# Kernel tuning notes

Hardware: AMD Instinct MI355X
Metric: run time of the kernel (lower is better)

The kernel has to match this reference:

```python
import jax, jax.numpy as jnp
import numpy as np

B, S, H = 2, 2048, 1024
I = 1024          # moe_intermediate_size
E = 8             # n_routed_experts
K = 2             # num_experts_per_tok
SCALE = 1.0       # routed_scaling_factor


def setup_inputs() -> dict:
    key = jax.random.key(0)
    ks = jax.random.split(key, 8)
    sd = 1.0 / np.sqrt(H)
    si = 1.0 / np.sqrt(I)
    return {
        "hidden_states": jax.random.normal(ks[0], (B, S, H), jnp.float32),
        "router_w": jax.random.uniform(ks[1], (E, H), jnp.float32, -sd, sd),
        # shared expert (n_shared_experts = 1); weights stored [in, out]
        "shared_gate": jax.random.uniform(ks[2], (H, I), jnp.float32, -sd, sd),
        "shared_up": jax.random.uniform(ks[3], (H, I), jnp.float32, -sd, sd),
        "shared_down": jax.random.uniform(ks[4], (I, H), jnp.float32, -si, si),
        # routed experts, stacked [E, in, out]
        "experts_gate": jax.random.uniform(ks[5], (E, H, I), jnp.float32, -sd, sd),
        "experts_up": jax.random.uniform(ks[6], (E, H, I), jnp.float32, -sd, sd),
        "experts_down": jax.random.uniform(ks[7], (E, I, H), jnp.float32, -si, si),
    }


def reference(hidden_states, router_w, shared_gate, shared_up, shared_down,
              experts_gate, experts_up, experts_down):
    residual = hidden_states
    x = hidden_states.reshape(-1, H)                      # [T, H], T = B*S

    # shared expert (SwiGLU-ish: sigmoid(gate) * up)
    sg = x @ shared_gate
    su = x @ shared_up
    shared_out = (jax.nn.sigmoid(sg) * su) @ shared_down  # [T, H]

    # router: softmax over experts, greedy top-k
    logits = x @ router_w.T                               # [T, E]
    scores = jax.nn.softmax(logits.astype(jnp.float32), axis=-1)
    topk_w, topk_idx = jax.lax.top_k(scores, K)           # [T, K]
    topk_w = topk_w * SCALE

    # dense compute of ALL experts on all tokens (faithful to reference)
    g = jnp.einsum('th,ehi->tei', x, experts_gate)        # [T, E, I]
    u = jnp.einsum('th,ehi->tei', x, experts_up)
    hid = jax.nn.sigmoid(g) * u
    expert_outputs = jnp.einsum('tei,eih->teh', hid, experts_down)  # [T, E, H]

    # gather top-k expert outputs and combine
    selected = jnp.take_along_axis(expert_outputs, topk_idx[:, :, None], axis=1)  # [T, K, H]
    routed_out = (selected * topk_w[:, :, None]).sum(axis=1)                      # [T, H]

    out = residual + (shared_out + routed_out).reshape(B, S, H)
    return out
```

## Files before the change

kernel.cpp:

```cpp
#include <hip/hip_runtime.h>
#include <hip/hip_bf16.h>

#define T_TOK 4096
#define HDIM 1024
#define IDIM 1024
#define EDIM 8

typedef __attribute__((ext_vector_type(8))) short bf16x8;
typedef __attribute__((ext_vector_type(4))) float f32x4;

static __device__ __forceinline__ unsigned short f2bf(float f) {
  union { float f; unsigned int u; } v; v.f = f;
  unsigned int u = v.u;
  unsigned int r = u + 0x7FFFu + ((u >> 16) & 1u);
  return (unsigned short)(r >> 16);
}

#define GLD16(g, l) __builtin_amdgcn_global_load_lds( \
    (const __attribute__((address_space(1))) void*)(g), \
    (__attribute__((address_space(3))) void*)(l), 16, 0, 0)

__global__ __launch_bounds__(256) void convert_x(const float4* __restrict__ x4,
                                                 ushort4* __restrict__ xb4) {
  int i = blockIdx.x * 256 + threadIdx.x;
  float4 v = x4[i];
  ushort4 o;
  o.x = f2bf(v.x); o.y = f2bf(v.y); o.z = f2bf(v.z); o.w = f2bf(v.w);
  xb4[i] = o;
}

__global__ void zero_cnt(int* __restrict__ cnt) {
  if (threadIdx.x < 16) cnt[threadIdx.x] = 0;
}

struct SrcPtrs { const float* p[6]; };

__global__ __launch_bounds__(256) void transpose_all(SrcPtrs S,
                                                     unsigned short* __restrict__ dstBase) {
  __shared__ unsigned short t[32][36];
  const int z = blockIdx.z;
  const float* src;
  if (z == 0)       src = S.p[0];
  else if (z == 1)  src = S.p[1];
  else if (z == 2)  src = S.p[2];
  else if (z < 11)  src = S.p[3] + (size_t)(z - 3)  * 1048576;
  else if (z < 19)  src = S.p[4] + (size_t)(z - 11) * 1048576;
  else              src = S.p[5] + (size_t)(z - 19) * 1048576;
  unsigned short* dst = dstBase + (size_t)z * 1048576;

  const int r0 = blockIdx.y * 32;
  const int c0 = blockIdx.x * 32;
  const int tid = threadIdx.x;
  const int rr = tid >> 3;
  const int cc = (tid & 7) * 4;
  const float4 v = *(const float4*)&src[(size_t)(r0 + rr) * 1024 + c0 + cc];
  t[rr][cc + 0] = f2bf(v.x); t[rr][cc + 1] = f2bf(v.y);
  t[rr][cc + 2] = f2bf(v.z); t[rr][cc + 3] = f2bf(v.w);
  __syncthreads();
  const int n = rr;
  const int k4 = cc;
  ushort4 o;
  o.x = t[k4 + 0][n]; o.y = t[k4 + 1][n]; o.z = t[k4 + 2][n]; o.w = t[k4 + 3][n];
  *(ushort4*)&dst[(size_t)(c0 + n) * 1024 + r0 + k4] = o;
}

__global__ __launch_bounds__(256) void router2(
    const float* __restrict__ x, const float* __restrict__ rw,
    int* __restrict__ cnt, int* __restrict__ list, float* __restrict__ wgt) {
  __shared__ float rwT[1024 * 8];
  const int tid = threadIdx.x;
#pragma unroll
  for (int c = 0; c < 4; c++) {
    const int h = c * 256 + tid;
    float v[8];
#pragma unroll
    for (int e = 0; e < EDIM; e++) v[e] = rw[e * 1024 + h];
    *(float4*)&rwT[h * 8]     = make_float4(v[0], v[1], v[2], v[3]);
    *(float4*)&rwT[h * 8 + 4] = make_float4(v[4], v[5], v[6], v[7]);
  }
  __syncthreads();

  const int tt = tid >> 4;
  const int pp = tid & 15;
  const int t = blockIdx.x * 16 + tt;
  const float* xr = x + (size_t)t * HDIM;

  float a[EDIM];
#pragma unroll
  for (int e = 0; e < EDIM; e++) a[e] = 0.f;

#pragma unroll 8
  for (int i = 0; i < 64; i++) {
    const int h = pp + 16 * i;
    const float xs = xr[h];
    const float4 r0 = *(const float4*)&rwT[h * 8];
    const float4 r1 = *(const float4*)&rwT[h * 8 + 4];
    a[0] += xs * r0.x; a[1] += xs * r0.y; a[2] += xs * r0.z; a[3] += xs * r0.w;
    a[4] += xs * r1.x; a[5] += xs * r1.y; a[6] += xs * r1.z; a[7] += xs * r1.w;
  }
#pragma unroll
  for (int s = 1; s < 16; s <<= 1) {
#pragma unroll
    for (int e = 0; e < EDIM; e++) a[e] += __shfl_xor(a[e], s, 16);
  }
  if (pp == 0) {
    float m = a[0];
#pragma unroll
    for (int e = 1; e < EDIM; e++) m = fmaxf(m, a[e]);
    float p[EDIM]; float s = 0.f;
#pragma unroll
    for (int e = 0; e < EDIM; e++) { p[e] = expf(a[e] - m); s += p[e]; }
    float inv = 1.f / s;
    int e1 = 0; float b1 = p[0];
#pragma unroll
    for (int e = 1; e < EDIM; e++) if (p[e] > b1) { b1 = p[e]; e1 = e; }
    int e2 = -1; float b2 = -1.f;
#pragma unroll
    for (int e = 0; e < EDIM; e++) if (e != e1 && p[e] > b2) { b2 = p[e]; e2 = e; }
    int pos1 = atomicAdd(&cnt[e1], 1);
    list[e1 * T_TOK + pos1] = t; wgt[e1 * T_TOK + pos1] = b1 * inv;
    int pos2 = atomicAdd(&cnt[e2], 1);
    list[e2 * T_TOK + pos2] = t; wgt[e2 * T_TOK + pos2] = b2 * inv;
  }
}

template <bool GATHER>
__global__ __launch_bounds__(256) void gateup_gemm(
    const unsigned short* __restrict__ xb,
    const unsigned short* __restrict__ WgT_, const unsigned short* __restrict__ WuT_,
    unsigned short* __restrict__ hid,
    const int* __restrict__ cnt, const int* __restrict__ list) {
  __shared__ unsigned short Al[128 * 64];
  __shared__ unsigned short Bg[64 * 64];
  __shared__ unsigned short Bu[64 * 64];

  const int tid = threadIdx.x;
  const int lane = tid & 63;
  const int w = tid >> 6;
  const int wm = w >> 1, wn = w & 1;

  int count, hidbase, e = 0;
  const unsigned short *wg, *wu;
  if constexpr (GATHER) {
    e = blockIdx.z;
    count = cnt[e];
    if ((int)blockIdx.y * 128 >= count) return;
    int off = 0;
#pragma unroll
    for (int i = 0; i < EDIM; i++) off += (i < e) ? cnt[i] : 0;
    hidbase = off;
    wg = WgT_ + (size_t)e * HDIM * IDIM;
    wu = WuT_ + (size_t)e * HDIM * IDIM;
  } else {
    count = T_TOK; hidbase = 0; wg = WgT_; wu = WuT_;
  }
  const int m0 = blockIdx.y * 128;
  const int n0 = blockIdx.x * 64;

  const unsigned short* gA[4];
  unsigned short* lA[4];
#pragma unroll
  for (int j = 0; j < 4; j++) {
    const int s = w * 256 + j * 64 + lane;
    const int row = s >> 3;
    const int cg = (s & 7) ^ (row & 7);
    int tok;
    if constexpr (GATHER) {
      int p = m0 + row; if (p >= count) p = count - 1;
      tok = list[e * T_TOK + p];
    } else {
      tok = m0 + row;
    }
    gA[j] = xb + (size_t)tok * HDIM + cg * 8;
    lA[j] = &Al[(w * 256 + j * 64) * 8];
  }
  const unsigned short *gG[2], *gU[2];
  unsigned short *lG[2], *lU[2];
#pragma unroll
  for (int j = 0; j < 2; j++) {
    const int s = w * 128 + j * 64 + lane;
    const int row = s >> 3;
    const int cg = (s & 7) ^ (row & 7);
    gG[j] = wg + (size_t)(n0 + row) * HDIM + cg * 8;
    gU[j] = wu + (size_t)(n0 + row) * HDIM + cg * 8;
    lG[j] = &Bg[(w * 128 + j * 64) * 8];
    lU[j] = &Bu[(w * 128 + j * 64) * 8];
  }

  f32x4 accg[4][2], accu[4][2];
  const f32x4 z4 = {0.f, 0.f, 0.f, 0.f};
#pragma unroll
  for (int i = 0; i < 4; i++)
#pragma unroll
    for (int j = 0; j < 2; j++) { accg[i][j] = z4; accu[i][j] = z4; }

  const int q = lane >> 4;
  const int r16 = lane & 15;
  const int rx = r16 & 7;

  for (int k0 = 0; k0 < HDIM; k0 += 64) {
    __syncthreads();
#pragma unroll
    for (int j = 0; j < 4; j++) GLD16(gA[j] + k0, lA[j]);
#pragma unroll
    for (int j = 0; j < 2; j++) { GLD16(gG[j] + k0, lG[j]); GLD16(gU[j] + k0, lU[j]); }
    __syncthreads();

    bf16x8 af[4][2], bg2[2][2], bu2[2][2];
#pragma unroll
    for (int h = 0; h < 2; h++) {
      const int ch = ((h * 4 + q) ^ rx) * 8;
#pragma unroll
      for (int i = 0; i < 4; i++)
        af[i][h] = *(const bf16x8*)&Al[(wm * 64 + i * 16 + r16) * 64 + ch];
#pragma unroll
      for (int j = 0; j < 2; j++) {
        bg2[j][h] = *(const bf16x8*)&Bg[(wn * 32 + j * 16 + r16) * 64 + ch];
        bu2[j][h] = *(const bf16x8*)&Bu[(wn * 32 + j * 16 + r16) * 64 + ch];
      }
    }
#pragma unroll
    for (int h = 0; h < 2; h++)
#pragma unroll
      for (int i = 0; i < 4; i++)
#pragma unroll
        for (int j = 0; j < 2; j++) {
          accg[i][j] = __builtin_amdgcn_mfma_f32_16x16x32_bf16(af[i][h], bg2[j][h], accg[i][j], 0, 0, 0);
          accu[i][j] = __builtin_amdgcn_mfma_f32_16x16x32_bf16(af[i][h], bu2[j][h], accu[i][j], 0, 0, 0);
        }
  }

#pragma unroll
  for (int i = 0; i < 4; i++) {
#pragma unroll
    for (int j = 0; j < 2; j++) {
      const int col = n0 + wn * 32 + j * 16 + r16;
#pragma unroll
      for (int r = 0; r < 4; r++) {
        int pos = m0 + wm * 64 + i * 16 + q * 4 + r;
        bool ok = GATHER ? (pos < count) : true;
        if (ok) {
          float g = accg[i][j][r], u = accu[i][j][r];
          float h = u / (1.f + __expf(-g));
          hid[(size_t)(hidbase + pos) * IDIM + col] = f2bf(h);
        }
      }
    }
  }
}

template <bool ROUTED>
__global__ __launch_bounds__(256) void down_gemm(
    const unsigned short* __restrict__ hidin,
    const unsigned short* __restrict__ WdT_,
    float* __restrict__ out, const float* __restrict__ resid,
    const int* __restrict__ cnt, const int* __restrict__ list,
    const float* __restrict__ wgt) {
  __shared__ unsigned short Al[128 * 64];
  __shared__ unsigned short Bl[128 * 64];

  const int tid = threadIdx.x;
  const int lane = tid & 63;
  const int w = tid >> 6;
  const int wm = w >> 1, wn = w & 1;

  int count, abase, e = 0;
  const unsigned short* wd;
  if constexpr (ROUTED) {
    e = blockIdx.z;
    count = cnt[e];
    if ((int)blockIdx.y * 128 >= count) return;
    int off = 0;
#pragma unroll
    for (int i = 0; i < EDIM; i++) off += (i < e) ? cnt[i] : 0;
    abase = off;
    wd = WdT_ + (size_t)e * IDIM * HDIM;
  } else {
    count = T_TOK; abase = 0; wd = WdT_;
  }
  const int m0 = blockIdx.y * 128;
  const int n0 = blockIdx.x * 128;

  const unsigned short *gA[4], *gB[4];
  unsigned short *lA[4], *lB[4];
#pragma unroll
  for (int j = 0; j < 4; j++) {
    const int s = w * 256 + j * 64 + lane;
    const int row = s >> 3;
    const int cg = (s & 7) ^ (row & 7);
    gA[j] = hidin + (size_t)(abase + m0 + row) * IDIM + cg * 8;
    gB[j] = wd + (size_t)(n0 + row) * IDIM + cg * 8;
    lA[j] = &Al[(w * 256 + j * 64) * 8];
    lB[j] = &Bl[(w * 256 + j * 64) * 8];
  }

  f32x4 acc[4][4];
  const f32x4 z4 = {0.f, 0.f, 0.f, 0.f};
#pragma unroll
  for (int i = 0; i < 4; i++)
#pragma unroll
    for (int j = 0; j < 4; j++) acc[i][j] = z4;

  const int q = lane >> 4;
  const int r16 = lane & 15;
  const int rx = r16 & 7;

  for (int k0 = 0; k0 < IDIM; k0 += 64) {
    __syncthreads();
#pragma unroll
    for (int j = 0; j < 4; j++) GLD16(gA[j] + k0, lA[j]);
#pragma unroll
    for (int j = 0; j < 4; j++) GLD16(gB[j] + k0, lB[j]);
    __syncthreads();

    bf16x8 af[4][2], bf4[4][2];
#pragma unroll
    for (int h = 0; h < 2; h++) {
      const int ch = ((h * 4 + q) ^ rx) * 8;
#pragma unroll
      for (int i = 0; i < 4; i++)
        af[i][h] = *(const bf16x8*)&Al[(wm * 64 + i * 16 + r16) * 64 + ch];
#pragma unroll
      for (int j = 0; j < 4; j++)
        bf4[j][h] = *(const bf16x8*)&Bl[(wn * 64 + j * 16 + r16) * 64 + ch];
    }
#pragma unroll
    for (int h = 0; h < 2; h++)
#pragma unroll
      for (int i = 0; i < 4; i++)
#pragma unroll
        for (int j = 0; j < 4; j++)
          acc[i][j] = __builtin_amdgcn_mfma_f32_16x16x32_bf16(af[i][h], bf4[j][h], acc[i][j], 0, 0, 0);
  }

#pragma unroll
  for (int i = 0; i < 4; i++) {
    int toks[4]; float ws4[4];
#pragma unroll
    for (int r = 0; r < 4; r++) {
      int pos = m0 + wm * 64 + i * 16 + q * 4 + r;
      if constexpr (ROUTED) {
        bool ok = pos < count;
        toks[r] = ok ? list[e * T_TOK + pos] : -1;
        ws4[r] = ok ? wgt[e * T_TOK + pos] : 0.f;
      } else {
        toks[r] = pos; ws4[r] = 1.f;
      }
    }
#pragma unroll
    for (int j = 0; j < 4; j++) {
      const int col = n0 + wn * 64 + j * 16 + r16;
#pragma unroll
      for (int r = 0; r < 4; r++) {
        if constexpr (ROUTED) {
          if (toks[r] >= 0)
            atomicAdd(&out[(size_t)toks[r] * HDIM + col], ws4[r] * acc[i][j][r]);
        } else {
          size_t idx = (size_t)toks[r] * HDIM + col;
          out[idx] = resid[idx] + acc[i][j][r];
        }
      }
    }
  }
}

extern "C" void kernel_launch(void* const* d_in, const int* in_sizes, int n_in,
                              void* d_out, int out_size, void* d_ws, size_t ws_size,
                              hipStream_t stream) {
  const float* x  = (const float*)d_in[0];
  const float* rw = (const float*)d_in[1];
  const float* sg = (const float*)d_in[2];
  const float* su = (const float*)d_in[3];
  const float* sd = (const float*)d_in[4];
  const float* eg = (const float*)d_in[5];
  const float* eu = (const float*)d_in[6];
  const float* ed = (const float*)d_in[7];
  float* out = (float*)d_out;

  char* ws = (char*)d_ws;
  unsigned short* xb   = (unsigned short*)ws;
  unsigned short* shid = xb + (size_t)T_TOK * HDIM;
  unsigned short* rhid = shid + (size_t)T_TOK * IDIM;
  int*   cnt  = (int*)(rhid + (size_t)(T_TOK * 2 + 128) * IDIM);
  int*   list = cnt + 16;
  float* wgt  = (float*)(list + EDIM * T_TOK);
  unsigned short* wT = (unsigned short*)(wgt + EDIM * T_TOK);
  unsigned short* sgT = wT;
  unsigned short* suT = sgT + (size_t)HDIM * IDIM;
  unsigned short* sdT = suT + (size_t)HDIM * IDIM;
  unsigned short* egT = sdT + (size_t)IDIM * HDIM;
  unsigned short* euT = egT + (size_t)EDIM * HDIM * IDIM;
  unsigned short* edT = euT + (size_t)EDIM * HDIM * IDIM;

  zero_cnt<<<1, 64, 0, stream>>>(cnt);
  convert_x<<<(T_TOK * HDIM) / 1024, 256, 0, stream>>>((const float4*)x, (ushort4*)xb);
  router2<<<T_TOK / 16, 256, 0, stream>>>(x, rw, cnt, list, wgt);

  SrcPtrs S; S.p[0] = sg; S.p[1] = su; S.p[2] = sd; S.p[3] = eg; S.p[4] = eu; S.p[5] = ed;
  transpose_all<<<dim3(32, 32, 27), 256, 0, stream>>>(S, wT);

  gateup_gemm<false><<<dim3(IDIM / 64, T_TOK / 128, 1), 256, 0, stream>>>(
      xb, sgT, suT, shid, nullptr, nullptr);
  gateup_gemm<true><<<dim3(IDIM / 64, T_TOK / 128, EDIM), 256, 0, stream>>>(
      xb, egT, euT, rhid, cnt, list);

  down_gemm<false><<<dim3(HDIM / 128, T_TOK / 128, 1), 256, 0, stream>>>(
      shid, sdT, out, x, nullptr, nullptr, nullptr);
  down_gemm<true><<<dim3(HDIM / 128, T_TOK / 128, EDIM), 256, 0, stream>>>(
      rhid, edT, out, nullptr, cnt, list, wgt);
}
```

Baseline: 391.1 us.

## Merge shared and routed expert GEMMs into single launches with double-buffered K=32 stages

Treats the shared expert as a ninth expert so gate/up and down each run as one grid launch instead of two, and reorders the transposed weight layout to match. The GEMM main loops now use a 2-stage LDS double buffer with 32-wide K slices, so the next tile's global-to-LDS loads overlap the current tile's MFMAs. The residual is copied into the output during x conversion, and the shared down GEMM now accumulates with atomics instead of plain stores. This removes launch gaps and exposed load latency, at the cost of more atomic traffic and smaller per-stage K tiles.

```diff
diff --git a/kernel.cpp b/kernel.cpp
--- a/kernel.cpp
+++ b/kernel.cpp
@@ -5,6 +5,7 @@
 #define HDIM 1024
 #define IDIM 1024
 #define EDIM 8
+#define HID_SHARED_BASE 8320
 
 typedef __attribute__((ext_vector_type(8))) short bf16x8;
 typedef __attribute__((ext_vector_type(4))) float f32x4;
@@ -21,9 +22,11 @@
     (__attribute__((address_space(3))) void*)(l), 16, 0, 0)
 
 __global__ __launch_bounds__(256) void convert_x(const float4* __restrict__ x4,
-                                                 ushort4* __restrict__ xb4) {
+                                                 ushort4* __restrict__ xb4,
+                                                 float4* __restrict__ out4) {
   int i = blockIdx.x * 256 + threadIdx.x;
   float4 v = x4[i];
+  out4[i] = v;
   ushort4 o;
   o.x = f2bf(v.x); o.y = f2bf(v.y); o.z = f2bf(v.z); o.w = f2bf(v.w);
   xb4[i] = o;
@@ -39,14 +42,14 @@
                                                      unsigned short* __restrict__ dstBase) {
   __shared__ unsigned short t[32][36];
   const int z = blockIdx.z;
-  const float* src;
-  if (z == 0)       src = S.p[0];
-  else if (z == 1)  src = S.p[1];
-  else if (z == 2)  src = S.p[2];
-  else if (z < 11)  src = S.p[3] + (size_t)(z - 3)  * 1048576;
-  else if (z < 19)  src = S.p[4] + (size_t)(z - 11) * 1048576;
-  else              src = S.p[5] + (size_t)(z - 19) * 1048576;
-  unsigned short* dst = dstBase + (size_t)z * 1048576;
+  const float* src; int dz;
+  if (z == 0)      { src = S.p[0];                              dz = 8;  }
+  else if (z == 1) { src = S.p[1];                              dz = 17; }
+  else if (z == 2) { src = S.p[2];                              dz = 26; }
+  else if (z < 11) { src = S.p[3] + (size_t)(z - 3)  * 1048576; dz = z - 3; }
+  else if (z < 19) { src = S.p[4] + (size_t)(z - 11) * 1048576; dz = 9 + (z - 11); }
+  else             { src = S.p[5] + (size_t)(z - 19) * 1048576; dz = 18 + (z - 19); }
+  unsigned short* dst = dstBase + (size_t)dz * 1048576;
 
   const int r0 = blockIdx.y * 32;
   const int c0 = blockIdx.x * 32;
@@ -57,11 +60,9 @@
   t[rr][cc + 0] = f2bf(v.x); t[rr][cc + 1] = f2bf(v.y);
   t[rr][cc + 2] = f2bf(v.z); t[rr][cc + 3] = f2bf(v.w);
   __syncthreads();
-  const int n = rr;
-  const int k4 = cc;
   ushort4 o;
-  o.x = t[k4 + 0][n]; o.y = t[k4 + 1][n]; o.z = t[k4 + 2][n]; o.w = t[k4 + 3][n];
-  *(ushort4*)&dst[(size_t)(c0 + n) * 1024 + r0 + k4] = o;
+  o.x = t[cc + 0][rr]; o.y = t[cc + 1][rr]; o.z = t[cc + 2][rr]; o.w = t[cc + 3][rr];
+  *(ushort4*)&dst[(size_t)(c0 + rr) * 1024 + r0 + cc] = o;
 }
 
 __global__ __launch_bounds__(256) void router2(
@@ -124,68 +125,57 @@
   }
 }
 
-template <bool GATHER>
-__global__ __launch_bounds__(256) void gateup_gemm(
+__global__ __launch_bounds__(256) void gateup_f(
     const unsigned short* __restrict__ xb,
-    const unsigned short* __restrict__ WgT_, const unsigned short* __restrict__ WuT_,
+    const unsigned short* __restrict__ gateT,
+    const unsigned short* __restrict__ upT,
     unsigned short* __restrict__ hid,
     const int* __restrict__ cnt, const int* __restrict__ list) {
-  __shared__ unsigned short Al[128 * 64];
-  __shared__ unsigned short Bg[64 * 64];
-  __shared__ unsigned short Bu[64 * 64];
+  __shared__ unsigned short Al[2][128 * 32];
+  __shared__ unsigned short Bg[2][64 * 32];
+  __shared__ unsigned short Bu[2][64 * 32];
 
   const int tid = threadIdx.x;
   const int lane = tid & 63;
   const int w = tid >> 6;
   const int wm = w >> 1, wn = w & 1;
-
-  int count, hidbase, e = 0;
-  const unsigned short *wg, *wu;
-  if constexpr (GATHER) {
-    e = blockIdx.z;
-    count = cnt[e];
-    if ((int)blockIdx.y * 128 >= count) return;
-    int off = 0;
-#pragma unroll
-    for (int i = 0; i < EDIM; i++) off += (i < e) ? cnt[i] : 0;
-    hidbase = off;
-    wg = WgT_ + (size_t)e * HDIM * IDIM;
-    wu = WuT_ + (size_t)e * HDIM * IDIM;
-  } else {
-    count = T_TOK; hidbase = 0; wg = WgT_; wu = WuT_;
-  }
+  const int z = blockIdx.z;
   const int m0 = blockIdx.y * 128;
   const int n0 = blockIdx.x * 64;
 
-  const unsigned short* gA[4];
-  unsigned short* lA[4];
-#pragma unroll
-  for (int j = 0; j < 4; j++) {
-    const int s = w * 256 + j * 64 + lane;
-    const int row = s >> 3;
-    const int cg = (s & 7) ^ (row & 7);
-    int tok;
-    if constexpr (GATHER) {
-      int p = m0 + row; if (p >= count) p = count - 1;
-      tok = list[e * T_TOK + p];
-    } else {
-      tok = m0 + row;
-    }
-    gA[j] = xb + (size_t)tok * HDIM + cg * 8;
-    lA[j] = &Al[(w * 256 + j * 64) * 8];
-  }
-  const unsigned short *gG[2], *gU[2];
-  unsigned short *lG[2], *lU[2];
+  int count, hidbase;
+  if (z < EDIM) {
+    count = cnt[z];
+    if (m0 >= count) return;
+    int off = 0;
+#pragma unroll
+    for (int i = 0; i < EDIM; i++) off += (i < z) ? cnt[i] : 0;
+    hidbase = off;
+  } else {
+    count = T_TOK;
+    hidbase = HID_SHARED_BASE;
+  }
+  const unsigned short* wg = gateT + (size_t)z * HDIM * IDIM;
+  const unsigned short* wu = upT   + (size_t)z * HDIM * IDIM;
+
+  const unsigned short* gA[2];
 #pragma unroll
   for (int j = 0; j < 2; j++) {
     const int s = w * 128 + j * 64 + lane;
-    const int row = s >> 3;
-    const int cg = (s & 7) ^ (row & 7);
-    gG[j] = wg + (size_t)(n0 + row) * HDIM + cg * 8;
-    gU[j] = wu + (size_t)(n0 + row) * HDIM + cg * 8;
-    lG[j] = &Bg[(w * 128 + j * 64) * 8];
-    lU[j] = &Bu[(w * 128 + j * 64) * 8];
-  }
+    const int row = s >> 2;
+    const int g = (s & 3) ^ ((row + (row >> 2)) & 3);
+    int tok;
+    if (z < EDIM) {
+      int p = m0 + row; if (p >= count) p = count - 1;
+      tok = list[z * T_TOK + p];
+    } else tok = m0 + row;
+    gA[j] = xb + (size_t)tok * HDIM + g * 8;
+  }
+  const int sB = w * 64 + lane;
+  const int rowB = sB >> 2;
+  const int gB = (sB & 3) ^ ((rowB + (rowB >> 2)) & 3);
+  const unsigned short* gGp = wg + (size_t)(n0 + rowB) * HDIM + gB * 8;
+  const unsigned short* gUp = wu + (size_t)(n0 + rowB) * HDIM + gB * 8;
 
   f32x4 accg[4][2], accu[4][2];
   const f32x4 z4 = {0.f, 0.f, 0.f, 0.f};
@@ -196,38 +186,42 @@
 
   const int q = lane >> 4;
   const int r16 = lane & 15;
-  const int rx = r16 & 7;
-
-  for (int k0 = 0; k0 < HDIM; k0 += 64) {
+  const int ch = (q ^ ((r16 + (r16 >> 2)) & 3)) * 8;
+
+  auto stage = [&](int k0, int b) {
+    GLD16(gA[0] + k0, &Al[b][(w * 128) * 8]);
+    GLD16(gA[1] + k0, &Al[b][(w * 128 + 64) * 8]);
+    GLD16(gGp + k0, &Bg[b][(w * 64) * 8]);
+    GLD16(gUp + k0, &Bu[b][(w * 64) * 8]);
+  };
+  auto compute = [&](int b) {
+    bf16x8 af[4], bg2[2], bu2[2];
+#pragma unroll
+    for (int i = 0; i < 4; i++)
+      af[i] = *(const bf16x8*)&Al[b][(wm * 64 + i * 16 + r16) * 32 + ch];
+#pragma unroll
+    for (int j = 0; j < 2; j++) {
+      bg2[j] = *(const bf16x8*)&Bg[b][(wn * 32 + j * 16 + r16) * 32 + ch];
+      bu2[j] = *(const bf16x8*)&Bu[b][(wn * 32 + j * 16 + r16) * 32 + ch];
+    }
+#pragma unroll
+    for (int i = 0; i < 4; i++)
+#pragma unroll
+      for (int j = 0; j < 2; j++) {
+        accg[i][j] = __builtin_amdgcn_mfma_f32_16x16x32_bf16(af[i], bg2[j], accg[i][j], 0, 0, 0);
+        accu[i][j] = __builtin_amdgcn_mfma_f32_16x16x32_bf16(af[i], bu2[j], accu[i][j], 0, 0, 0);
+      }
+  };
+
+  stage(0, 0);
+#pragma unroll 1
+  for (int p = 0; p < 16; p++) {
     __syncthreads();
-#pragma unroll
-    for (int j = 0; j < 4; j++) GLD16(gA[j] + k0, lA[j]);
-#pragma unroll
-    for (int j = 0; j < 2; j++) { GLD16(gG[j] + k0, lG[j]); GLD16(gU[j] + k0, lU[j]); }
+    stage((2 * p + 1) * 32, 1);
+    compute(0);
     __syncthreads();
-
-    bf16x8 af[4][2], bg2[2][2], bu2[2][2];
-#pragma unroll
-    for (int h = 0; h < 2; h++) {
-      const int ch = ((h * 4 + q) ^ rx) * 8;
-#pragma unroll
-      for (int i = 0; i < 4; i++)
-        af[i][h] = *(const bf16x8*)&Al[(wm * 64 + i * 16 + r16) * 64 + ch];
-#pragma unroll
-      for (int j = 0; j < 2; j++) {
-        bg2[j][h] = *(const bf16x8*)&Bg[(wn * 32 + j * 16 + r16) * 64 + ch];
-        bu2[j][h] = *(const bf16x8*)&Bu[(wn * 32 + j * 16 + r16) * 64 + ch];
-      }
-    }
-#pragma unroll
-    for (int h = 0; h < 2; h++)
-#pragma unroll
-      for (int i = 0; i < 4; i++)
-#pragma unroll
-        for (int j = 0; j < 2; j++) {
-          accg[i][j] = __builtin_amdgcn_mfma_f32_16x16x32_bf16(af[i][h], bg2[j][h], accg[i][j], 0, 0, 0);
-          accu[i][j] = __builtin_amdgcn_mfma_f32_16x16x32_bf16(af[i][h], bu2[j][h], accu[i][j], 0, 0, 0);
-        }
+    if (p < 15) stage((2 * p + 2) * 32, 0);
+    compute(1);
   }
 
 #pragma unroll
@@ -238,8 +232,7 @@
 #pragma unroll
       for (int r = 0; r < 4; r++) {
         int pos = m0 + wm * 64 + i * 16 + q * 4 + r;
-        bool ok = GATHER ? (pos < count) : true;
-        if (ok) {
+        if (pos < count) {
           float g = accg[i][j][r], u = accu[i][j][r];
           float h = u / (1.f + __expf(-g));
           hid[(size_t)(hidbase + pos) * IDIM + col] = f2bf(h);
@@ -249,49 +242,45 @@
   }
 }
 
-template <bool ROUTED>
-__global__ __launch_bounds__(256) void down_gemm(
-    const unsigned short* __restrict__ hidin,
-    const unsigned short* __restrict__ WdT_,
-    float* __restrict__ out, const float* __restrict__ resid,
+__global__ __launch_bounds__(256) void down_f(
+    const unsigned short* __restrict__ hid,
+    const unsigned short* __restrict__ downT,
+    float* __restrict__ out,
     const int* __restrict__ cnt, const int* __restrict__ list,
     const float* __restrict__ wgt) {
-  __shared__ unsigned short Al[128 * 64];
-  __shared__ unsigned short Bl[128 * 64];
+  __shared__ unsigned short Al[2][128 * 32];
+  __shared__ unsigned short Bl[2][128 * 32];
 
   const int tid = threadIdx.x;
   const int lane = tid & 63;
   const int w = tid >> 6;
   const int wm = w >> 1, wn = w & 1;
-
-  int count, abase, e = 0;
-  const unsigned short* wd;
-  if constexpr (ROUTED) {
-    e = blockIdx.z;
-    count = cnt[e];
-    if ((int)blockIdx.y * 128 >= count) return;
-    int off = 0;
-#pragma unroll
-    for (int i = 0; i < EDIM; i++) off += (i < e) ? cnt[i] : 0;
-    abase = off;
-    wd = WdT_ + (size_t)e * IDIM * HDIM;
-  } else {
-    count = T_TOK; abase = 0; wd = WdT_;
-  }
+  const int z = blockIdx.z;
   const int m0 = blockIdx.y * 128;
   const int n0 = blockIdx.x * 128;
 
-  const unsigned short *gA[4], *gB[4];
-  unsigned short *lA[4], *lB[4];
-#pragma unroll
-  for (int j = 0; j < 4; j++) {
-    const int s = w * 256 + j * 64 + lane;
-    const int row = s >> 3;
-    const int cg = (s & 7) ^ (row & 7);
-    gA[j] = hidin + (size_t)(abase + m0 + row) * IDIM + cg * 8;
-    gB[j] = wd + (size_t)(n0 + row) * IDIM + cg * 8;
-    lA[j] = &Al[(w * 256 + j * 64) * 8];
-    lB[j] = &Bl[(w * 256 + j * 64) * 8];
+  int count, abase;
+  if (z < EDIM) {
+    count = cnt[z];
+    if (m0 >= count) return;
+    int off = 0;
+#pragma unroll
+    for (int i = 0; i < EDIM; i++) off += (i < z) ? cnt[i] : 0;
+    abase = off;
+  } else {
+    count = T_TOK;
+    abase = HID_SHARED_BASE;
+  }
+  const unsigned short* wd = downT + (size_t)z * IDIM * HDIM;
+
+  const unsigned short *gA[2], *gBp[2];
+#pragma unroll
+  for (int j = 0; j < 2; j++) {
+    const int s = w * 128 + j * 64 + lane;
+    const int row = s >> 2;
+    const int g = (s & 3) ^ ((row + (row >> 2)) & 3);
+    gA[j]  = hid + (size_t)(abase + m0 + row) * IDIM + g * 8;
+    gBp[j] = wd + (size_t)(n0 + row) * IDIM + g * 8;
   }
 
   f32x4 acc[4][4];
@@ -303,34 +292,38 @@
 
   const int q = lane >> 4;
   const int r16 = lane & 15;
-  const int rx = r16 & 7;
-
-  for (int k0 = 0; k0 < IDIM; k0 += 64) {
+  const int ch = (q ^ ((r16 + (r16 >> 2)) & 3)) * 8;
+
+  auto stage = [&](int k0, int b) {
+    GLD16(gA[0] + k0,  &Al[b][(w * 128) * 8]);
+    GLD16(gA[1] + k0,  &Al[b][(w * 128 + 64) * 8]);
+    GLD16(gBp[0] + k0, &Bl[b][(w * 128) * 8]);
+    GLD16(gBp[1] + k0, &Bl[b][(w * 128 + 64) * 8]);
+  };
+  auto compute = [&](int b) {
+    bf16x8 af[4], bf4[4];
+#pragma unroll
+    for (int i = 0; i < 4; i++)
+      af[i] = *(const bf16x8*)&Al[b][(wm * 64 + i * 16 + r16) * 32 + ch];
+#pragma unroll
+    for (int j = 0; j < 4; j++)
+      bf4[j] = *(const bf16x8*)&Bl[b][(wn * 64 + j * 16 + r16) * 32 + ch];
+#pragma unroll
+    for (int i = 0; i < 4; i++)
+#pragma unroll
+      for (int j = 0; j < 4; j++)
+        acc[i][j] = __builtin_amdgcn_mfma_f32_16x16x32_bf16(af[i], bf4[j], acc[i][j], 0, 0, 0);
+  };
+
+  stage(0, 0);
+#pragma unroll 1
+  for (int p = 0; p < 16; p++) {
     __syncthreads();
-#pragma unroll
-    for (int j = 0; j < 4; j++) GLD16(gA[j] + k0, lA[j]);
-#pragma unroll
-    for (int j = 0; j < 4; j++) GLD16(gB[j] + k0, lB[j]);
+    stage((2 * p + 1) * 32, 1);
+    compute(0);
     __syncthreads();
-
-    bf16x8 af[4][2], bf4[4][2];
-#pragma unroll
-    for (int h = 0; h < 2; h++) {
-      const int ch = ((h * 4 + q) ^ rx) * 8;
-#pragma unroll
-      for (int i = 0; i < 4; i++)
-        af[i][h] = *(const bf16x8*)&Al[(wm * 64 + i * 16 + r16) * 64 + ch];
-#pragma unroll
-      for (int j = 0; j < 4; j++)
-        bf4[j][h] = *(const bf16x8*)&Bl[(wn * 64 + j * 16 + r16) * 64 + ch];
-    }
-#pragma unroll
-    for (int h = 0; h < 2; h++)
-#pragma unroll
-      for (int i = 0; i < 4; i++)
-#pragma unroll
-        for (int j = 0; j < 4; j++)
-          acc[i][j] = __builtin_amdgcn_mfma_f32_16x16x32_bf16(af[i][h], bf4[j][h], acc[i][j], 0, 0, 0);
+    if (p < 15) stage((2 * p + 2) * 32, 0);
+    compute(1);
   }
 
 #pragma unroll
@@ -339,10 +332,10 @@
 #pragma unroll
     for (int r = 0; r < 4; r++) {
       int pos = m0 + wm * 64 + i * 16 + q * 4 + r;
-      if constexpr (ROUTED) {
+      if (z < EDIM) {
         bool ok = pos < count;
-        toks[r] = ok ? list[e * T_TOK + pos] : -1;
-        ws4[r] = ok ? wgt[e * T_TOK + pos] : 0.f;
+        toks[r] = ok ? list[z * T_TOK + pos] : -1;
+        ws4[r] = ok ? wgt[z * T_TOK + pos] : 0.f;
       } else {
         toks[r] = pos; ws4[r] = 1.f;
       }
@@ -352,13 +345,8 @@
       const int col = n0 + wn * 64 + j * 16 + r16;
 #pragma unroll
       for (int r = 0; r < 4; r++) {
-        if constexpr (ROUTED) {
-          if (toks[r] >= 0)
-            atomicAdd(&out[(size_t)toks[r] * HDIM + col], ws4[r] * acc[i][j][r]);
-        } else {
-          size_t idx = (size_t)toks[r] * HDIM + col;
-          out[idx] = resid[idx] + acc[i][j][r];
-        }
+        if (toks[r] >= 0)
+          atomicAdd(&out[(size_t)toks[r] * HDIM + col], ws4[r] * acc[i][j][r]);
       }
     }
   }
@@ -378,34 +366,24 @@
   float* out = (float*)d_out;
 
   char* ws = (char*)d_ws;
-  unsigned short* xb   = (unsigned short*)ws;
-  unsigned short* shid = xb + (size_t)T_TOK * HDIM;
-  unsigned short* rhid = shid + (size_t)T_TOK * IDIM;
-  int*   cnt  = (int*)(rhid + (size_t)(T_TOK * 2 + 128) * IDIM);
+  unsigned short* xb  = (unsigned short*)ws;
+  unsigned short* hid = xb + (size_t)T_TOK * HDIM;
+  int*   cnt  = (int*)(hid + (size_t)(HID_SHARED_BASE + T_TOK) * IDIM);
   int*   list = cnt + 16;
   float* wgt  = (float*)(list + EDIM * T_TOK);
-  unsigned short* wT = (unsigned short*)(wgt + EDIM * T_TOK);
-  unsigned short* sgT = wT;
-  unsigned short* suT = sgT + (size_t)HDIM * IDIM;
-  unsigned short* sdT = suT + (size_t)HDIM * IDIM;
-  unsigned short* egT = sdT + (size_t)IDIM * HDIM;
-  unsigned short* euT = egT + (size_t)EDIM * HDIM * IDIM;
-  unsigned short* edT = euT + (size_t)EDIM * HDIM * IDIM;
+  unsigned short* wT    = (unsigned short*)(wgt + EDIM * T_TOK);
+  unsigned short* gateT = wT;
+  unsigned short* upT   = wT + (size_t)9 * 1048576;
+  unsigned short* downT = wT + (size_t)18 * 1048576;
 
   zero_cnt<<<1, 64, 0, stream>>>(cnt);
-  convert_x<<<(T_TOK * HDIM) / 1024, 256, 0, stream>>>((const float4*)x, (ushort4*)xb);
+  convert_x<<<(T_TOK * HDIM) / 1024, 256, 0, stream>>>(
+      (const float4*)x, (ushort4*)xb, (float4*)out);
   router2<<<T_TOK / 16, 256, 0, stream>>>(x, rw, cnt, list, wgt);
 
   SrcPtrs S; S.p[0] = sg; S.p[1] = su; S.p[2] = sd; S.p[3] = eg; S.p[4] = eu; S.p[5] = ed;
   transpose_all<<<dim3(32, 32, 27), 256, 0, stream>>>(S, wT);
 
-  gateup_gemm<false><<<dim3(IDIM / 64, T_TOK / 128, 1), 256, 0, stream>>>(
-      xb, sgT, suT, shid, nullptr, nullptr);
-  gateup_gemm<true><<<dim3(IDIM / 64, T_TOK / 128, EDIM), 256, 0, stream>>>(
-      xb, egT, euT, rhid, cnt, list);
-
-  down_gemm<false><<<dim3(HDIM / 128, T_TOK / 128, 1), 256, 0, stream>>>(
-      shid, sdT, out, x, nullptr, nullptr, nullptr);
-  down_gemm<true><<<dim3(HDIM / 128, T_TOK / 128, EDIM), 256, 0, stream>>>(
-      rhid, edT, out, nullptr, cnt, list, wgt);
-}
+  gateup_f<<<dim3(IDIM / 64, 32, 9), 256, 0, stream>>>(xb, gateT, upT, hid, cnt, list);
+  down_f<<<dim3(HDIM / 128, 32, 9), 256, 0, stream>>>(hid, downT, out, cnt, list, wgt);
+}
```

Measured after the change: 386.8 us. About the same (-1.1%).
